# Performance work log

Measured on AMD Instinct MI355X. Metric: run time of the kernel, lower is better.

The kernel has to match this reference:

```python
import jax, jax.numpy as jnp
import numpy as np
import math

NUM_HEADS = 16
VEC_SIZE = 1024
HEAD_DIM = VEC_SIZE // NUM_HEADS


def setup_inputs() -> dict:
    key = jax.random.key(0)
    k1, k2, k3, k4, k5 = jax.random.split(key, 5)
    B, S, D = 2, 2048, VEC_SIZE
    x = jax.random.normal(k1, (B, S, D), dtype=jnp.float32)
    # Linear params, torch-style: y = x @ W.T + b
    s1 = 1.0 / math.sqrt(D)
    W_qkv = jax.random.uniform(k2, (3 * D, D), minval=-s1, maxval=s1, dtype=jnp.float32)
    b_qkv = jax.random.uniform(k3, (3 * D,), minval=-s1, maxval=s1, dtype=jnp.float32)
    W_out = jax.random.uniform(k4, (D, D), minval=-s1, maxval=s1, dtype=jnp.float32)
    b_out = jax.random.uniform(k5, (D,), minval=-s1, maxval=s1, dtype=jnp.float32)
    return {"x": x, "W_qkv": W_qkv, "b_qkv": b_qkv, "W_out": W_out, "b_out": b_out}


def reference(x, W_qkv, b_qkv, W_out, b_out):
    B, S, D = x.shape
    H, Hd = NUM_HEADS, HEAD_DIM
    qkv = x @ W_qkv.T + b_qkv                      # [B,S,3D]
    q, k, v = jnp.split(qkv, 3, axis=-1)
    # [B,S,H,Hd] -> [B,H,S,Hd]
    q = q.reshape(B, S, H, Hd).transpose(0, 2, 1, 3)
    k = k.reshape(B, S, H, Hd).transpose(0, 2, 1, 3)
    v = v.reshape(B, S, H, Hd).transpose(0, 2, 1, 3)
    weight = jnp.einsum('bhqd,bhkd->bhqk', q, k)   # [B,H,S,S]
    causal = jnp.triu(jnp.ones((S, S), dtype=bool), k=1)
    weight = jnp.where(causal, -jnp.inf, weight)
    weight = weight / jnp.sqrt(jnp.asarray(Hd, dtype=weight.dtype))
    weight = jax.nn.softmax(weight, axis=-1)
    out = jnp.einsum('bhqk,bhkd->bhqd', weight, v)  # [B,H,S,Hd]
    out = out.transpose(0, 2, 1, 3).reshape(B, S, D)
    return out @ W_out.T + b_out
```

## Files before the change

kernel.cpp:

```cpp
#include <hip/hip_runtime.h>
#include <hip/hip_bf16.h>

typedef __attribute__((ext_vector_type(8))) short short8;
typedef __attribute__((ext_vector_type(4))) short s4v;
typedef __attribute__((ext_vector_type(4))) float floatx4;

__device__ inline floatx4 mfma_bf16(short8 a, short8 b, floatx4 c) {
  return __builtin_amdgcn_mfma_f32_16x16x32_bf16(a, b, c, 0, 0, 0);
}
__device__ inline float exp2_fast(float x) { return __builtin_amdgcn_exp2f(x); }

__device__ inline short bf16s(float f) {
  __hip_bfloat16 h = __float2bfloat16(f);
  return *reinterpret_cast<short*>(&h);
}
__device__ inline float sbf16(short s) {
  return __bfloat162float(*reinterpret_cast<__hip_bfloat16*>(&s));
}

__device__ inline void gld16(__hip_bfloat16* lds, const __hip_bfloat16* g) {
  __builtin_amdgcn_global_load_lds(
      (const __attribute__((address_space(1))) void*)g,
      (__attribute__((address_space(3))) void*)lds, 16, 0, 0);
}

__global__ __launch_bounds__(256) void cvt_all(
    const float* __restrict__ x, const float* __restrict__ wqkv,
    const float* __restrict__ wout, __hip_bfloat16* __restrict__ xb,
    __hip_bfloat16* __restrict__ wqkvb, __hip_bfloat16* __restrict__ wob) {
  const int n1 = 4194304, n2 = 3145728;
  int i = (blockIdx.x * 256 + threadIdx.x) * 8;
  const float* src;
  __hip_bfloat16* dst;
  int off;
  if (i < n1) { src = x; dst = xb; off = i; }
  else if (i < n1 + n2) { src = wqkv; dst = wqkvb; off = i - n1; }
  else { src = wout; dst = wob; off = i - n1 - n2; }
  float4 a = *reinterpret_cast<const float4*>(src + off);
  float4 b = *reinterpret_cast<const float4*>(src + off + 4);
  __hip_bfloat16 t[8];
  t[0] = __float2bfloat16(a.x); t[1] = __float2bfloat16(a.y);
  t[2] = __float2bfloat16(a.z); t[3] = __float2bfloat16(a.w);
  t[4] = __float2bfloat16(b.x); t[5] = __float2bfloat16(b.y);
  t[6] = __float2bfloat16(b.z); t[7] = __float2bfloat16(b.w);
  *reinterpret_cast<short8*>(dst + off) = *reinterpret_cast<short8*>(t);
}

__device__ inline void stage_half(__hip_bfloat16* lds, const __hip_bfloat16* g,
                                  int K, int tid) {
#pragma unroll
  for (int it = 0; it < 2; ++it) {
    int idx = it * 512 + tid;
    int row = idx >> 3, col = ((idx & 7) ^ (row & 7)) * 8;
    gld16(lds + idx * 8, g + (size_t)row * K + col);
  }
}
__device__ inline void stage_q(__hip_bfloat16* lds, const __hip_bfloat16* g,
                               int K, int tid) {
  int row = tid >> 3, col = ((tid & 7) ^ (row & 7)) * 8;
  gld16(lds + tid * 8, g + (size_t)row * K + col);
}

#define VMW(N) asm volatile("s_waitcnt vmcnt(" #N ")" ::: "memory")
#define BAR __builtin_amdgcn_s_barrier()

#define LDA8(dst, BUF, MH)                                                     \
  do {                                                                         \
    _Pragma("unroll") for (int mf = 0; mf < 4; ++mf) {                         \
      int rh = wm * 64 + mf * 16 + l15;                                        \
      _Pragma("unroll") for (int ks = 0; ks < 2; ++ks)                         \
          dst[mf][ks] = *reinterpret_cast<const short8*>(                      \
              &SA[BUF][MH][rh * 64 + (((ks * 4 + quad) ^ (rh & 7)) * 8)]);     \
    }                                                                          \
  } while (0)
#define LDB4(dst, BUF, NH)                                                     \
  do {                                                                         \
    _Pragma("unroll") for (int nf = 0; nf < 2; ++nf) {                         \
      int rh = wn * 32 + nf * 16 + l15;                                        \
      _Pragma("unroll") for (int ks = 0; ks < 2; ++ks)                         \
          dst[nf][ks] = *reinterpret_cast<const short8*>(                      \
              &SB[BUF][NH][rh * 64 + (((ks * 4 + quad) ^ (rh & 7)) * 8)]);     \
    }                                                                          \
  } while (0)
#define MM16(MH, NH, AF, BF)                                                   \
  do {                                                                         \
    _Pragma("unroll") for (int mf = 0; mf < 4; ++mf)                           \
        _Pragma("unroll") for (int nf = 0; nf < 2; ++nf) {                     \
      acc[MH][NH][mf][nf] = mfma_bf16(AF[mf][0], BF[nf][0], acc[MH][NH][mf][nf]); \
      acc[MH][NH][mf][nf] = mfma_bf16(AF[mf][1], BF[nf][1], acc[MH][NH][mf][nf]); \
    }                                                                          \
  } while (0)
#define PH(RD, STG, MH, NH, AF, BF, WT)                                        \
  do {                                                                         \
    RD;                                                                        \
    STG;                                                                       \
    BAR;                                                                       \
    __builtin_amdgcn_s_setprio(1);                                             \
    MM16(MH, NH, AF, BF);                                                      \
    __builtin_amdgcn_s_setprio(0);                                             \
    WT;                                                                        \
    BAR;                                                                       \
  } while (0)

template<bool OUT_BF16>
__global__ __launch_bounds__(512, 2) void gemm_256(
    const __hip_bfloat16* __restrict__ A, const __hip_bfloat16* __restrict__ Bt,
    const float* __restrict__ bias, void* __restrict__ Cout,
    int M, int N, int K) {
  __shared__ __align__(16) __hip_bfloat16 SA[2][2][128 * 64];
  __shared__ __align__(16) __hip_bfloat16 SB[2][2][128 * 64];
  const int tid = threadIdx.x;
  const int lane = tid & 63, quad = (lane >> 4), l15 = lane & 15;
  const int wave = tid >> 6;
  const int wm = wave >> 2, wn = wave & 3;

  const int nbx = gridDim.x;
  int bid = blockIdx.y * nbx + blockIdx.x;
  const int nwg = nbx * gridDim.y;
  if ((nwg & 7) == 0) bid = (bid & 7) * (nwg >> 3) + (bid >> 3);
  const int bx = bid % nbx, by = bid / nbx;
  const int m0 = by * 256, n0 = bx * 256;

  const __hip_bfloat16* Abase = A + (size_t)m0 * K;
  const __hip_bfloat16* Bbase = Bt + (size_t)n0 * K;
  const int NT = K >> 6;

  floatx4 acc[2][2][4][2];
#pragma unroll
  for (int a = 0; a < 2; ++a)
#pragma unroll
    for (int b = 0; b < 2; ++b)
#pragma unroll
      for (int c = 0; c < 4; ++c)
#pragma unroll
        for (int d = 0; d < 2; ++d) acc[a][b][c][d] = (floatx4){0.f, 0.f, 0.f, 0.f};

  short8 af0[4][2], af1[4][2];
  short8 bf0[2][2], bf1[2][2];

  stage_half(&SA[0][0][0], Abase, K, tid);
  stage_half(&SB[0][0][0], Bbase, K, tid);
  stage_half(&SA[0][1][0], Abase + (size_t)128 * K, K, tid);
  stage_half(&SB[0][1][0], Bbase + (size_t)128 * K, K, tid);
  stage_half(&SA[1][0][0], Abase + 64, K, tid);
  stage_half(&SB[1][0][0], Bbase + 64, K, tid);
  stage_half(&SA[1][1][0], Abase + (size_t)128 * K + 64, K, tid);
  stage_half(&SB[1][1][0], Bbase + (size_t)128 * K + 64, K, tid);
  VMW(12);
  BAR;

  for (int t = 0; t <= NT - 3; ++t) {
    const int cb = t & 1;
    const size_t k2 = (size_t)(t + 2) * 64;
    PH({ LDA8(af0, cb, 0); LDB4(bf0, cb, 0); }, (void)0,
       0, 0, af0, bf0, VMW(10));
    PH(LDA8(af1, cb, 1),
       { stage_half(&SA[cb][0][0], Abase + k2, K, tid);
         stage_half(&SB[cb][0][0], Bbase + k2, K, tid); },
       1, 0, af1, bf0, VMW(12));
    PH(LDB4(bf1, cb, 1),
       stage_half(&SA[cb][1][0], Abase + (size_t)128 * K + k2, K, tid),
       1, 1, af1, bf1, (void)0);
    PH((void)0,
       stage_half(&SB[cb][1][0], Bbase + (size_t)128 * K + k2, K, tid),
       0, 1, af0, bf1, VMW(12));
  }
  {
    const int cb = (NT - 2) & 1;
    PH({ LDA8(af0, cb, 0); LDB4(bf0, cb, 0); }, (void)0, 0, 0, af0, bf0, VMW(10));
    PH(LDA8(af1, cb, 1), (void)0, 1, 0, af1, bf0, VMW(8));
    PH(LDB4(bf1, cb, 1), (void)0, 1, 1, af1, bf1, (void)0);
    PH((void)0, (void)0, 0, 1, af0, bf1, VMW(4));
  }
  {
    const int cb = (NT - 1) & 1;
    PH({ LDA8(af0, cb, 0); LDB4(bf0, cb, 0); }, (void)0, 0, 0, af0, bf0, VMW(2));
    PH(LDA8(af1, cb, 1), (void)0, 1, 0, af1, bf0, VMW(0));
    LDB4(bf1, cb, 1);
    __builtin_amdgcn_s_setprio(1);
    MM16(1, 1, af1, bf1);
    MM16(0, 1, af0, bf1);
    __builtin_amdgcn_s_setprio(0);
  }

#pragma unroll
  for (int nh = 0; nh < 2; ++nh)
#pragma unroll
    for (int nf = 0; nf < 2; ++nf) {
      int gn = n0 + nh * 128 + wn * 32 + nf * 16 + l15;
      float bv = bias[gn];
#pragma unroll
      for (int mh = 0; mh < 2; ++mh)
#pragma unroll
        for (int mf = 0; mf < 4; ++mf)
#pragma unroll
          for (int rg = 0; rg < 4; ++rg) {
            int gm = m0 + mh * 128 + wm * 64 + mf * 16 + quad * 4 + rg;
            float v = acc[mh][nh][mf][nf][rg] + bv;
            if (OUT_BF16)
              ((__hip_bfloat16*)Cout)[(size_t)gm * N + gn] = __float2bfloat16(v);
            else
              ((float*)Cout)[(size_t)gm * N + gn] = v;
          }
    }
}

__global__ __launch_bounds__(512, 2) void gemm_n64(
    const __hip_bfloat16* __restrict__ A, const __hip_bfloat16* __restrict__ Bt,
    const float* __restrict__ bias, float* __restrict__ Cout,
    int M, int N, int K) {
  __shared__ __align__(16) __hip_bfloat16 SA[2][2][128 * 64];
  __shared__ __align__(16) __hip_bfloat16 SB[2][64 * 64];
  const int tid = threadIdx.x;
  const int lane = tid & 63, quad = (lane >> 4), l15 = lane & 15;
  const int wave = tid >> 6;
  const int wm = wave >> 2, wn = wave & 3;

  const int nbx = gridDim.x;
  int bid = blockIdx.y * nbx + blockIdx.x;
  const int nwg = nbx * gridDim.y;
  if ((nwg & 7) == 0) bid = (bid & 7) * (nwg >> 3) + (bid >> 3);
  const int bx = bid % nbx, by = bid / nbx;
  const int m0 = by * 256, n0 = bx * 64;

  const __hip_bfloat16* Abase = A + (size_t)m0 * K;
  const __hip_bfloat16* Bbase = Bt + (size_t)n0 * K;
  const int NT = K >> 6;

  floatx4 acc[2][4];
#pragma unroll
  for (int a = 0; a < 2; ++a)
#pragma unroll
    for (int c = 0; c < 4; ++c) acc[a][c] = (floatx4){0.f, 0.f, 0.f, 0.f};

  short8 af0[4][2], af1[4][2];
  short8 bf[2];

#define N64_LDA(dst, BUF, MH)                                                  \
  do {                                                                         \
    _Pragma("unroll") for (int mf = 0; mf < 4; ++mf) {                         \
      int rh = wm * 64 + mf * 16 + l15;                                        \
      _Pragma("unroll") for (int ks = 0; ks < 2; ++ks)                         \
          dst[mf][ks] = *reinterpret_cast<const short8*>(                      \
              &SA[BUF][MH][rh * 64 + (((ks * 4 + quad) ^ (rh & 7)) * 8)]);     \
    }                                                                          \
  } while (0)
#define N64_LDB(BUF)                                                           \
  do {                                                                         \
    int rh = wn * 16 + l15;                                                    \
    _Pragma("unroll") for (int ks = 0; ks < 2; ++ks)                           \
        bf[ks] = *reinterpret_cast<const short8*>(                             \
            &SB[BUF][rh * 64 + (((ks * 4 + quad) ^ (rh & 7)) * 8)]);           \
  } while (0)
#define N64_MM(MH, AF)                                                         \
  do {                                                                         \
    _Pragma("unroll") for (int mf = 0; mf < 4; ++mf) {                         \
      acc[MH][mf] = mfma_bf16(AF[mf][0], bf[0], acc[MH][mf]);                  \
      acc[MH][mf] = mfma_bf16(AF[mf][1], bf[1], acc[MH][mf]);                  \
    }                                                                          \
  } while (0)
#define N64_PH(RD, STG, MH, AF, WT)                                            \
  do {                                                                         \
    RD;                                                                        \
    STG;                                                                       \
    BAR;                                                                       \
    __builtin_amdgcn_s_setprio(1);                                             \
    N64_MM(MH, AF);                                                            \
    __builtin_amdgcn_s_setprio(0);                                             \
    WT;                                                                        \
    BAR;                                                                       \
  } while (0)

  stage_half(&SA[0][0][0], Abase, K, tid);
  stage_q(&SB[0][0], Bbase, K, tid);
  stage_half(&SA[0][1][0], Abase + (size_t)128 * K, K, tid);
  stage_half(&SA[1][0][0], Abase + 64, K, tid);
  stage_q(&SB[1][0], Bbase + 64, K, tid);
  VMW(5);
  BAR;

  for (int t = 0; t <= NT - 3; ++t) {
    const int cb = t & 1, nb = cb ^ 1;
    const size_t k1 = (size_t)(t + 1) * 64, k2 = (size_t)(t + 2) * 64;
    N64_PH({ N64_LDA(af0, cb, 0); N64_LDB(cb); },
           stage_half(&SA[nb][1][0], Abase + (size_t)128 * K + k1, K, tid),
           0, af0, VMW(5));
    N64_PH(N64_LDA(af1, cb, 1),
           { stage_half(&SA[cb][0][0], Abase + k2, K, tid);
             stage_q(&SB[cb][0], Bbase + k2, K, tid); },
           1, af1, VMW(5));
  }
  {
    const int cb = (NT - 2) & 1, nb = cb ^ 1;
    const size_t k1 = (size_t)(NT - 1) * 64;
    N64_PH({ N64_LDA(af0, cb, 0); N64_LDB(cb); },
           stage_half(&SA[nb][1][0], Abase + (size_t)128 * K + k1, K, tid),
           0, af0, VMW(5));
    N64_PH(N64_LDA(af1, cb, 1), (void)0, 1, af1, VMW(2));
  }
  {
    const int cb = (NT - 1) & 1;
    N64_PH({ N64_LDA(af0, cb, 0); N64_LDB(cb); }, (void)0, 0, af0, VMW(0));
    N64_LDA(af1, cb, 1);
    __builtin_amdgcn_s_setprio(1);
    N64_MM(1, af1);
    __builtin_amdgcn_s_setprio(0);
  }

  {
    int gn = n0 + wn * 16 + l15;
    float bv = bias[gn];
#pragma unroll
    for (int mh = 0; mh < 2; ++mh)
#pragma unroll
      for (int mf = 0; mf < 4; ++mf)
#pragma unroll
        for (int rg = 0; rg < 4; ++rg) {
          int gm = m0 + mh * 128 + wm * 64 + mf * 16 + quad * 4 + rg;
          Cout[(size_t)gm * N + gn] = acc[mh][mf][rg] + bv;
        }
  }
#undef N64_LDA
#undef N64_LDB
#undef N64_MM
#undef N64_PH
}

__global__ __launch_bounds__(256, 4) void flash_attn(
    const __hip_bfloat16* __restrict__ qkv, __hip_bfloat16* __restrict__ out) {
  const int S = 2048, QKV = 3072;
  const int bx = blockIdx.x;
  const int g = (blockIdx.y >> 3) + 2 * blockIdx.z;
  int qt;
  if (g == 0)      qt = bx;
  else if (g == 1) qt = 31 - bx;
  else if (g == 2) qt = (bx + 8) & 31;
  else             qt = (23 - bx) & 31;
  const int h = blockIdx.y, b = blockIdx.z;
  const int q0 = qt * 64;
  __shared__ __align__(16) short Ps[2][64 * 64];
  const int tid = threadIdx.x;
  const int wave = tid >> 6, lane = tid & 63, quad = lane >> 4, l15 = lane & 15;
  const int rx = l15 & 7;
  const __hip_bfloat16* base = qkv + (size_t)b * S * QKV;
  const float c2 = 0.18033688011112042f;
  const floatx4 zero4 = {0.f, 0.f, 0.f, 0.f};
  const int krow = 16 * wave + l15;

  const __hip_bfloat16* kbase = base + 1024 + h * 64;
  const __hip_bfloat16* vbase = base + 2048 + h * 64;

  for (int it = 0; it < 2; ++it) {
    int v = tid + it * 256;
    int row = v >> 3, cb = v & 7;
    int colp = (cb ^ (row & 7)) * 8;
    short8 qv = *reinterpret_cast<const short8*>(
        base + (size_t)(q0 + row) * QKV + h * 64 + cb * 8);
    short qs[8];
    for (int e = 0; e < 8; ++e) qs[e] = bf16s(sbf16(qv[e]) * c2);
    *reinterpret_cast<short8*>(&Ps[1][row * 64 + colp]) = *reinterpret_cast<short8*>(qs);
  }
  short8 kA0 = *reinterpret_cast<const short8*>(
      kbase + (size_t)krow * QKV + quad * 8);
  short8 kA1 = *reinterpret_cast<const short8*>(
      kbase + (size_t)krow * QKV + 32 + quad * 8);
  __syncthreads();

  short8 aq[4][2];
  for (int t4 = 0; t4 < 4; ++t4)
    for (int s = 0; s < 2; ++s)
      aq[t4][s] = *reinterpret_cast<const short8*>(
          &Ps[1][(t4 * 16 + l15) * 64 + (((s * 4 + quad) ^ rx) * 8)]);

  floatx4 o_acc[4];
  for (int m = 0; m < 4; ++m) o_acc[m] = zero4;
  float lsum4[4] = {0.f, 0.f, 0.f, 0.f};
  short8 vA0, vA1;

  for (int j = 0; j <= qt; ++j) {
    const int cj = j & 1, pj = cj ^ 1;

    short8 kB0, kB1, vB0, vB1;
    if (j < qt) {
      const __hip_bfloat16* kp = kbase + (size_t)((j + 1) * 64 + krow) * QKV;
      kB0 = *reinterpret_cast<const short8*>(kp + quad * 8);
      kB1 = *reinterpret_cast<const short8*>(kp + 32 + quad * 8);
    }
    {
      const __hip_bfloat16* vp = vbase + (size_t)(j * 64 + quad * 8) * QKV + krow;
      for (int i = 0; i < 8; ++i) {
        vB0[i] = *reinterpret_cast<const short*>(vp + (size_t)i * QKV);
        vB1[i] = *reinterpret_cast<const short*>(vp + (size_t)(32 + i) * QKV);
      }
    }

    if (j > 0) {
      for (int s = 0; s < 2; ++s) {
        short8 bv = s ? vA1 : vA0;
        for (int m = 0; m < 4; ++m) {
          short8 ap = *reinterpret_cast<const short8*>(
              &Ps[pj][(m * 16 + l15) * 64 + (((4 * s + quad) ^ rx) * 8)]);
          o_acc[m] = mfma_bf16(ap, bv, o_acc[m]);
        }
      }
    }

    floatx4 sc[4];
    for (int t4 = 0; t4 < 4; ++t4) {
      sc[t4] = mfma_bf16(kA0, aq[t4][0], zero4);
      sc[t4] = mfma_bf16(kA1, aq[t4][1], sc[t4]);
    }
    if (j == qt) {
      int kloc = 16 * wave + quad * 4;
      for (int t4 = 0; t4 < 4; ++t4)
        for (int rg = 0; rg < 4; ++rg)
          if (kloc + rg > t4 * 16 + l15) sc[t4][rg] = -1e30f;
    }

    const int pcol = ((2 * wave + (quad >> 1)) ^ rx) * 8 + (quad & 1) * 4;
    for (int t4 = 0; t4 < 4; ++t4) {
      short pp[4];
      for (int rg = 0; rg < 4; ++rg) {
        float p = exp2_fast(sc[t4][rg]);
        lsum4[t4] += p;
        pp[rg] = bf16s(p);
      }
      *reinterpret_cast<s4v*>(&Ps[cj][(t4 * 16 + l15) * 64 + pcol]) =
          *reinterpret_cast<s4v*>(pp);
    }

    kA0 = kB0; kA1 = kB1; vA0 = vB0; vA1 = vB1;
    __syncthreads();
  }

  const int pq = qt & 1;
  for (int s = 0; s < 2; ++s) {
    short8 bv = s ? vA1 : vA0;
    for (int m = 0; m < 4; ++m) {
      short8 ap = *reinterpret_cast<const short8*>(
          &Ps[pq][(m * 16 + l15) * 64 + (((4 * s + quad) ^ rx) * 8)]);
      o_acc[m] = mfma_bf16(ap, bv, o_acc[m]);
    }
  }
  for (int t4 = 0; t4 < 4; ++t4) {
    lsum4[t4] += __shfl_xor(lsum4[t4], 16);
    lsum4[t4] += __shfl_xor(lsum4[t4], 32);
  }
  float* Lf = (float*)&Ps[pq ^ 1][0];
  if (quad == 0)
    for (int t4 = 0; t4 < 4; ++t4)
      Lf[wave * 64 + t4 * 16 + l15] = lsum4[t4];
  __syncthreads();
  if (tid < 64)
    Lf[256 + tid] = 1.0f / (Lf[tid] + Lf[64 + tid] + Lf[128 + tid] + Lf[192 + tid]);
  __syncthreads();

  const int dcol = h * 64 + krow;
  for (int m = 0; m < 4; ++m)
    for (int rg = 0; rg < 4; ++rg) {
      int q = m * 16 + quad * 4 + rg;
      out[(size_t)(b * S + q0 + q) * 1024 + dcol] =
          __float2bfloat16(o_acc[m][rg] * Lf[256 + q]);
    }
}

extern "C" void kernel_launch(void* const* d_in, const int* in_sizes, int n_in,
                              void* d_out, int out_size, void* d_ws, size_t ws_size,
                              hipStream_t stream) {
  const float* x    = (const float*)d_in[0];
  const float* Wqkv = (const float*)d_in[1];
  const float* bqkv = (const float*)d_in[2];
  const float* Wout = (const float*)d_in[3];
  const float* bout = (const float*)d_in[4];
  float* out = (float*)d_out;

  const int BS = 2 * 2048;
  const int D = 1024;
  char* ws = (char*)d_ws;
  __hip_bfloat16* xb    = (__hip_bfloat16*)(ws);
  __hip_bfloat16* wqkvb = (__hip_bfloat16*)(ws + (size_t)8  * 1048576);
  __hip_bfloat16* wob   = (__hip_bfloat16*)(ws + (size_t)14 * 1048576);
  __hip_bfloat16* qkvb  = (__hip_bfloat16*)(ws + (size_t)16 * 1048576);
  __hip_bfloat16* attnb = (__hip_bfloat16*)(ws + (size_t)40 * 1048576);

  cvt_all<<<4096, 256, 0, stream>>>(x, Wqkv, Wout, xb, wqkvb, wob);

  gemm_256<true><<<dim3(3072 / 256, BS / 256), 512, 0, stream>>>(
      xb, wqkvb, bqkv, qkvb, BS, 3 * D, D);

  flash_attn<<<dim3(32, 16, 2), 256, 0, stream>>>(qkvb, attnb);

  gemm_n64<<<dim3(1024 / 64, BS / 256), 512, 0, stream>>>(
      attnb, wob, bout, out, BS, D, D);
}
```

Baseline: 170.2 us.

## Triple-buffer gemm_n64 pipeline and drop mid-phase barrier in gemm_256

gemm_n64 moves from a two-phase double-buffered loop to a three-stage LDS ring. Each iteration reads the fragments for the current buffer, issues global-to-LDS loads two tiles ahead, runs all MFMAs, then waits and synchronizes once, so there are fewer barriers per K step. This raises LDS use for gemm_n64. The diff also removes a barrier inside the gemm_256 phase macro, which may cause races between LDS staging and fragment reads, and lowers the flash_attn launch-bounds occupancy hint from 4 to 3.

Result: no change. 168.2 us (median of 2 runs) (-1.2%).

```diff
diff --git a/kernel.cpp b/kernel.cpp
--- a/kernel.cpp
+++ b/kernel.cpp
@@ -94,7 +94,6 @@
   do {                                                                         \
     RD;                                                                        \
     STG;                                                                       \
-    BAR;                                                                       \
     __builtin_amdgcn_s_setprio(1);                                             \
     MM16(MH, NH, AF, BF);                                                      \
     __builtin_amdgcn_s_setprio(0);                                             \
@@ -209,8 +208,8 @@
     const __hip_bfloat16* __restrict__ A, const __hip_bfloat16* __restrict__ Bt,
     const float* __restrict__ bias, float* __restrict__ Cout,
     int M, int N, int K) {
-  __shared__ __align__(16) __hip_bfloat16 SA[2][2][128 * 64];
-  __shared__ __align__(16) __hip_bfloat16 SB[2][64 * 64];
+  __shared__ __align__(16) __hip_bfloat16 SA[3][2][128 * 64];
+  __shared__ __align__(16) __hip_bfloat16 SB[3][64 * 64];
   const int tid = threadIdx.x;
   const int lane = tid & 63, quad = (lane >> 4), l15 = lane & 15;
   const int wave = tid >> 6;
@@ -259,50 +258,52 @@
       acc[MH][mf] = mfma_bf16(AF[mf][1], bf[1], acc[MH][mf]);                  \
     }                                                                          \
   } while (0)
-#define N64_PH(RD, STG, MH, AF, WT)                                            \
-  do {                                                                         \
-    RD;                                                                        \
-    STG;                                                                       \
-    BAR;                                                                       \
-    __builtin_amdgcn_s_setprio(1);                                             \
-    N64_MM(MH, AF);                                                            \
-    __builtin_amdgcn_s_setprio(0);                                             \
-    WT;                                                                        \
-    BAR;                                                                       \
-  } while (0)
 
   stage_half(&SA[0][0][0], Abase, K, tid);
+  stage_half(&SA[0][1][0], Abase + (size_t)128 * K, K, tid);
   stage_q(&SB[0][0], Bbase, K, tid);
-  stage_half(&SA[0][1][0], Abase + (size_t)128 * K, K, tid);
   stage_half(&SA[1][0][0], Abase + 64, K, tid);
+  stage_half(&SA[1][1][0], Abase + (size_t)128 * K + 64, K, tid);
   stage_q(&SB[1][0], Bbase + 64, K, tid);
   VMW(5);
   BAR;
 
+  int cb = 0, sb = 2;
   for (int t = 0; t <= NT - 3; ++t) {
-    const int cb = t & 1, nb = cb ^ 1;
-    const size_t k1 = (size_t)(t + 1) * 64, k2 = (size_t)(t + 2) * 64;
-    N64_PH({ N64_LDA(af0, cb, 0); N64_LDB(cb); },
-           stage_half(&SA[nb][1][0], Abase + (size_t)128 * K + k1, K, tid),
-           0, af0, VMW(5));
-    N64_PH(N64_LDA(af1, cb, 1),
-           { stage_half(&SA[cb][0][0], Abase + k2, K, tid);
-             stage_q(&SB[cb][0], Bbase + k2, K, tid); },
-           1, af1, VMW(5));
+    const size_t k2 = (size_t)(t + 2) * 64;
+    N64_LDA(af0, cb, 0);
+    N64_LDA(af1, cb, 1);
+    N64_LDB(cb);
+    stage_half(&SA[sb][0][0], Abase + k2, K, tid);
+    stage_half(&SA[sb][1][0], Abase + (size_t)128 * K + k2, K, tid);
+    stage_q(&SB[sb][0], Bbase + k2, K, tid);
+    __builtin_amdgcn_s_setprio(1);
+    N64_MM(0, af0);
+    N64_MM(1, af1);
+    __builtin_amdgcn_s_setprio(0);
+    VMW(5);
+    BAR;
+    cb = (cb == 2) ? 0 : cb + 1;
+    sb = (sb == 2) ? 0 : sb + 1;
   }
   {
-    const int cb = (NT - 2) & 1, nb = cb ^ 1;
-    const size_t k1 = (size_t)(NT - 1) * 64;
-    N64_PH({ N64_LDA(af0, cb, 0); N64_LDB(cb); },
-           stage_half(&SA[nb][1][0], Abase + (size_t)128 * K + k1, K, tid),
-           0, af0, VMW(5));
-    N64_PH(N64_LDA(af1, cb, 1), (void)0, 1, af1, VMW(2));
+    N64_LDA(af0, cb, 0);
+    N64_LDA(af1, cb, 1);
+    N64_LDB(cb);
+    __builtin_amdgcn_s_setprio(1);
+    N64_MM(0, af0);
+    N64_MM(1, af1);
+    __builtin_amdgcn_s_setprio(0);
+    VMW(0);
+    BAR;
+    cb = (cb == 2) ? 0 : cb + 1;
   }
   {
-    const int cb = (NT - 1) & 1;
-    N64_PH({ N64_LDA(af0, cb, 0); N64_LDB(cb); }, (void)0, 0, af0, VMW(0));
+    N64_LDA(af0, cb, 0);
     N64_LDA(af1, cb, 1);
+    N64_LDB(cb);
     __builtin_amdgcn_s_setprio(1);
+    N64_MM(0, af0);
     N64_MM(1, af1);
     __builtin_amdgcn_s_setprio(0);
   }
@@ -323,10 +324,9 @@
 #undef N64_LDA
 #undef N64_LDB
 #undef N64_MM
-#undef N64_PH
-}
-
-__global__ __launch_bounds__(256, 4) void flash_attn(
+}
+
+__global__ __launch_bounds__(256, 3) void flash_attn(
     const __hip_bfloat16* __restrict__ qkv, __hip_bfloat16* __restrict__ out) {
   const int S = 2048, QKV = 3072;
   const int bx = blockIdx.x;
```
